# Kernel optimization log

Measured on AMD Instinct MI355X. Metric: run time of the kernel, lower is better.

The kernel has to match this reference:

```python
import jax, jax.numpy as jnp
import numpy as np

LAMBDA_TEMP = 20.0
GAMMA = 20.0
MARGIN = 0.05
EPS = 1e-8

B, K, M, D = 128, 256, 8, 128


def _unit(x, axis=-1):
    return x / jnp.linalg.norm(x, axis=axis, keepdims=True)


def setup_inputs() -> dict:
    key = jax.random.key(0)
    k1, k2, k3 = jax.random.split(key, 3)
    v_proj = _unit(jax.random.normal(k1, (B, K, D), dtype=jnp.float32))
    prototypes = _unit(jax.random.normal(k2, (K, M, D), dtype=jnp.float32))
    concept_labels = jax.random.randint(k3, (B, K), 0, 2, dtype=jnp.int64)
    return {"v_proj": v_proj, "concept_labels": concept_labels, "prototypes": prototypes}


def reference(v_proj, concept_labels, prototypes):
    # all-pairs prototype similarities: query vector (b,k) vs prototypes of concept c
    # sims: (B, K, C, M)
    sims = jnp.einsum('bkd,cmd->bkcm', v_proj, prototypes)
    # Eq.6: soft assignment over the M prototypes of each concept
    q = jax.nn.softmax(GAMMA * sims, axis=-1)
    # Eq.7-8: weighted similarity sim_c(v)  -> (B, K, C)
    sim = jnp.sum(q * sims, axis=-1)
    # positive similarity: concept k queried against its own prototypes, plus margin
    sim_pos = jnp.einsum('bkk->bk', sim) + MARGIN  # (B, K)
    # Eq.9: -log( exp(lam*sim_pos) / (sum_c exp(lam*sim_c) + eps) )
    denom = jnp.sum(jnp.exp(LAMBDA_TEMP * sim), axis=-1) + EPS  # (B, K)
    loss_bk = jnp.log(denom) - LAMBDA_TEMP * sim_pos  # (B, K)
    mask = (concept_labels == 1).astype(loss_bk.dtype)
    num_pos = jnp.sum(mask)
    total = jnp.sum(loss_bk * mask)
    return jnp.where(num_pos > 0, total / num_pos, total)
```

## Files before the change

### kernel.cpp

```cpp
#include <hip/hip_runtime.h>

#define LT      20.0f
#define LN2     0.69314718055994531f
#define C2EXP   28.853900817779268f
#define CHUNKS  16
#define NBLK    512

typedef _Float16 half8 __attribute__((ext_vector_type(8)));
typedef float    f32x4 __attribute__((ext_vector_type(4)));

#if __has_builtin(__builtin_amdgcn_exp2f)
#define EXP2F(x) __builtin_amdgcn_exp2f(x)
#else
#define EXP2F(x) __expf(0.69314718055994531f * (x))
#endif

__device__ __forceinline__ float swz16(float x) {
    return __int_as_float(__builtin_amdgcn_ds_swizzle(__float_as_int(x), 0x401F));
}

#define GLD16(gp, lp) __builtin_amdgcn_global_load_lds( \
    (const __attribute__((address_space(1))) void*)(gp), \
    (__attribute__((address_space(3))) void*)(lp), 16, 0, 0)

__global__ __launch_bounds__(256)
void mpcl_prep(const float* __restrict__ P, _Float16* __restrict__ Pw)
{
    int t    = blockIdx.x * 256 + threadIdx.x;
    int gcol = t >> 4;
    int dblk = t & 15;
    const float* src = P + ((size_t)gcol << 7) + dblk * 8;
    float4 a = *(const float4*)src;
    float4 b = *(const float4*)(src + 4);

    int ch   = gcol >> 7, col  = gcol & 127;
    int colq = col >> 5,  col5 = col & 31;
    int g = col5 >> 3, p = col5 & 7;
    int n = (g << 2) | (p & 3), h = p >> 2;
    int c = dblk >> 2, q = dblk & 3;
    int lane  = (q << 4) | n;
    int cfrag = (h << 2) | c;
    int slot  = ch * 2048 + colq * 512 + cfrag * 64 + lane;

    half8 hv;
    hv[0] = (_Float16)(C2EXP * a.x); hv[1] = (_Float16)(C2EXP * a.y);
    hv[2] = (_Float16)(C2EXP * a.z); hv[3] = (_Float16)(C2EXP * a.w);
    hv[4] = (_Float16)(C2EXP * b.x); hv[5] = (_Float16)(C2EXP * b.y);
    hv[6] = (_Float16)(C2EXP * b.z); hv[7] = (_Float16)(C2EXP * b.w);
    *(half8*)(Pw + (size_t)slot * 8) = hv;
}

__global__ __launch_bounds__(1024, 8)
void mpcl_main(const float* __restrict__ V,
               const int*   __restrict__ labels,
               const _Float16* __restrict__ Pw,
               float* __restrict__ part)
{
    __shared__ __align__(16) _Float16 Pst[2][2048 * 8];
    __shared__ float sh_denom[64];
    __shared__ float sh_simpos[64];

    const int tid  = threadIdx.x;
    const int lane = tid & 63;
    const int w    = tid >> 6;
    const int colq = w & 3;
    const int rg   = w >> 2;
    const int n    = lane & 15;
    const int q    = lane >> 4;
    const int rowbase = blockIdx.x * 64;

    if (tid < 64) { sh_denom[tid] = 0.0f; sh_simpos[tid] = 0.0f; }

    int lab = 0;
    if (tid < 64) lab = labels[rowbase + tid];

    const _Float16* gbase = Pw + (size_t)(w * 128 + lane) * 8;

#define STAGE(CH, B) do {                                       \
    const _Float16* g_ = gbase + (size_t)(CH) * 16384;          \
    _Float16* l_ = &Pst[B][(w * 128) * 8];                      \
    GLD16(g_,       l_);                                        \
    GLD16(g_ + 512, l_ + 512);                                  \
} while (0)

    half8 vh[4];
    {
        const float* vr = V + ((size_t)(rowbase + rg * 16 + n) << 7) + q * 8;
#pragma unroll
        for (int c = 0; c < 4; ++c) {
            float4 x0 = *(const float4*)(vr + c * 32);
            float4 x1 = *(const float4*)(vr + c * 32 + 4);
            vh[c][0] = (_Float16)x0.x; vh[c][1] = (_Float16)x0.y;
            vh[c][2] = (_Float16)x0.z; vh[c][3] = (_Float16)x0.w;
            vh[c][4] = (_Float16)x1.x; vh[c][5] = (_Float16)x1.y;
            vh[c][6] = (_Float16)x1.z; vh[c][7] = (_Float16)x1.w;
        }
    }
    __syncthreads();

    STAGE(0, 0);
    STAGE(1, 1);

    const int rowk = (rowbase + rg * 16 + n) & 255;
    const int aoff = (colq * 512 + lane) * 8;

    float dn = 0.f;
    int cA = colq * 4 + q;

#pragma unroll 1
    for (int ch = 0; ch < CHUNKS; ++ch) {
        if (ch < CHUNKS - 1) asm volatile("s_waitcnt vmcnt(2)" ::: "memory");
        else                 asm volatile("s_waitcnt vmcnt(0)" ::: "memory");
        __builtin_amdgcn_s_barrier();

        const _Float16* base = &Pst[ch & 1][0];

        f32x4 acc1 = {0.f, 0.f, 0.f, 0.f};
        f32x4 acc2 = {0.f, 0.f, 0.f, 0.f};
#pragma unroll
        for (int c = 0; c < 4; ++c) {
            half8 a1 = *(const half8*)&base[aoff + c * 512];
            half8 a2 = *(const half8*)&base[aoff + c * 512 + 2048];
            acc1 = __builtin_amdgcn_mfma_f32_16x16x32_f16(a1, vh[c], acc1, 0, 0, 0);
            acc2 = __builtin_amdgcn_mfma_f32_16x16x32_f16(a2, vh[c], acc2, 0, 0, 0);
        }

        asm volatile("s_waitcnt lgkmcnt(0)" ::: "memory");
        __builtin_amdgcn_s_barrier();
        if (ch + 2 < CHUNKS) STAGE(ch + 2, ch & 1);

        {
            float x0 = acc1[0], x1 = acc1[1], x2 = acc1[2], x3 = acc1[3];
            float x4 = acc2[0], x5 = acc2[1], x6 = acc2[2], x7 = acc2[3];
            float e0 = EXP2F(x0), e1 = EXP2F(x1), e2 = EXP2F(x2), e3 = EXP2F(x3);
            float e4 = EXP2F(x4), e5 = EXP2F(x5), e6 = EXP2F(x6), e7 = EXP2F(x7);
            float es = ((e0 + e1) + (e2 + e3)) + ((e4 + e5) + (e6 + e7));
            float ss = fmaf(e0, x0, fmaf(e1, x1, fmaf(e2, x2, e3 * x3)))
                     + fmaf(e4, x4, fmaf(e5, x5, fmaf(e6, x6, e7 * x7)));
            float simY = __fdividef(ss, es);
            dn += EXP2F(simY);
            if (cA == rowk)
                sh_simpos[rg * 16 + n] = simY;
        }
        cA += 16;
    }

    {
        float t = dn;
        t += swz16(t);
        t += __shfl_xor(t, 32);
        if (lane < 16)
            atomicAdd(&sh_denom[rg * 16 + n], t);
    }
    __syncthreads();

    if (w == 0) {
        float lp = logf(sh_denom[lane] + 1e-8f) - LN2 * sh_simpos[lane] - 1.0f;
        float mk = (lab == 1) ? 1.0f : 0.0f;
        float s  = lp * mk;
        float cc = mk;
#pragma unroll
        for (int off = 32; off >= 1; off >>= 1) {
            s  += __shfl_down(s, off);
            cc += __shfl_down(cc, off);
        }
        if (lane == 0) {
            part[2 * blockIdx.x]     = s;
            part[2 * blockIdx.x + 1] = cc;
        }
    }
}

__global__ __launch_bounds__(512)
void mpcl_finish(const float* __restrict__ part, float* __restrict__ out)
{
    __shared__ float sh[16];
    const int tid  = threadIdx.x;
    const int lane = tid & 63;
    const int w    = tid >> 6;

    float s  = part[2 * tid];
    float cc = part[2 * tid + 1];
#pragma unroll
    for (int off = 32; off >= 1; off >>= 1) {
        s  += __shfl_down(s, off);
        cc += __shfl_down(cc, off);
    }
    if (lane == 0) { sh[w] = s; sh[8 + w] = cc; }
    __syncthreads();
    if (tid == 0) {
        float ts = 0.f, tc = 0.f;
#pragma unroll
        for (int i = 0; i < 8; ++i) { ts += sh[i]; tc += sh[8 + i]; }
        out[0] = (tc > 0.0f) ? (ts / tc) : ts;
    }
}

extern "C" void kernel_launch(void* const* d_in, const int* in_sizes, int n_in,
                              void* d_out, int out_size, void* d_ws, size_t ws_size,
                              hipStream_t stream)
{
    const float* V      = (const float*)d_in[0];
    const int*   labels = (const int*)d_in[1];
    const float* P      = (const float*)d_in[2];
    float* out  = (float*)d_out;
    float* part = (float*)d_ws;
    _Float16* Pw = (_Float16*)((char*)d_ws + 16384);

    mpcl_prep<<<128, 256, 0, stream>>>(P, Pw);
    mpcl_main<<<NBLK, 1024, 0, stream>>>(V, labels, Pw, part);
    mpcl_finish<<<1, 512, 0, stream>>>(part, out);
}
```

Baseline: 97.21 us.

## Compact positive-label rows and run main kernel only on them

Adds a single-block compaction kernel that ballots over the labels, prefix-sums the positive rows into an index list and writes their count. The main kernel then processes only those rows through the index list, with 32 rows per 512-thread block. Blocks past the positive count exit early, so masked-out rows no longer pay for the prototype matmul and exponentials. The cost is an extra kernel launch with a serial scan, and an indirect gather of V rows.

Result: faster. 93.68 us (-3.6%).

```diff
diff --git a/kernel.cpp b/kernel.cpp
--- a/kernel.cpp
+++ b/kernel.cpp
@@ -4,7 +4,7 @@
 #define LN2     0.69314718055994531f
 #define C2EXP   28.853900817779268f
 #define CHUNKS  16
-#define NBLK    512
+#define NBLK    1024
 
 typedef _Float16 half8 __attribute__((ext_vector_type(8)));
 typedef float    f32x4 __attribute__((ext_vector_type(4)));
@@ -50,15 +50,69 @@
     *(half8*)(Pw + (size_t)slot * 8) = hv;
 }
 
-__global__ __launch_bounds__(1024, 8)
+__global__ __launch_bounds__(1024)
+void mpcl_compact(const int* __restrict__ labels, int* __restrict__ ridx,
+                  int* __restrict__ npos)
+{
+    __shared__ int wcnt[512];
+    __shared__ int wsum[8];
+    __shared__ int sbase[512];
+    __shared__ int tot;
+    const int tid = threadIdx.x, lane = tid & 63, w = tid >> 6;
+
+    int lab[32];
+#pragma unroll
+    for (int i = 0; i < 32; ++i) lab[i] = labels[i * 1024 + tid];
+#pragma unroll
+    for (int i = 0; i < 32; ++i) {
+        unsigned long long m = __ballot(lab[i] == 1);
+        if (lane == 0) wcnt[i * 16 + w] = __popcll(m);
+    }
+    __syncthreads();
+
+    int v = 0, orig = 0;
+    if (tid < 512) { v = wcnt[tid]; orig = v; }
+#pragma unroll
+    for (int off = 1; off < 64; off <<= 1) {
+        int t = __shfl_up(v, off);
+        if (lane >= off) v += t;
+    }
+    if (lane == 63 && w < 8) wsum[w] = v;
+    __syncthreads();
+    if (tid == 0) {
+        int acc = 0;
+#pragma unroll
+        for (int i = 0; i < 8; ++i) { int t = wsum[i]; wsum[i] = acc; acc += t; }
+        tot = acc; npos[0] = acc;
+    }
+    __syncthreads();
+    if (tid < 512) sbase[tid] = v - orig + wsum[w];
+    __syncthreads();
+
+#pragma unroll
+    for (int i = 0; i < 32; ++i) {
+        unsigned long long m = __ballot(lab[i] == 1);
+        int pos = sbase[i * 16 + w] + __popcll(m & ((1ull << lane) - 1));
+        if (lab[i] == 1) ridx[pos] = i * 1024 + tid;
+    }
+    for (int j = tot + tid; j < 32768; j += 1024) ridx[j] = 0;
+}
+
+__global__ __attribute__((amdgpu_flat_work_group_size(512, 512),
+                          amdgpu_waves_per_eu(4, 4)))
 void mpcl_main(const float* __restrict__ V,
-               const int*   __restrict__ labels,
                const _Float16* __restrict__ Pw,
+               const int* __restrict__ ridx,
+               const int* __restrict__ npos,
                float* __restrict__ part)
 {
     __shared__ __align__(16) _Float16 Pst[2][2048 * 8];
-    __shared__ float sh_denom[64];
-    __shared__ float sh_simpos[64];
+    __shared__ float sh_denom[32];
+    __shared__ float sh_simpos[32];
+
+    const int np = *npos;
+    const int rowbase = blockIdx.x * 32;
+    if (rowbase >= np) return;
 
     const int tid  = threadIdx.x;
     const int lane = tid & 63;
@@ -67,25 +121,24 @@
     const int rg   = w >> 2;
     const int n    = lane & 15;
     const int q    = lane >> 4;
-    const int rowbase = blockIdx.x * 64;
-
-    if (tid < 64) { sh_denom[tid] = 0.0f; sh_simpos[tid] = 0.0f; }
-
-    int lab = 0;
-    if (tid < 64) lab = labels[rowbase + tid];
-
-    const _Float16* gbase = Pw + (size_t)(w * 128 + lane) * 8;
+
+    if (tid < 32) { sh_denom[tid] = 0.0f; sh_simpos[tid] = 0.0f; }
+
+    const _Float16* gbase = Pw + (size_t)(w * 256 + lane) * 8;
 
 #define STAGE(CH, B) do {                                       \
     const _Float16* g_ = gbase + (size_t)(CH) * 16384;          \
-    _Float16* l_ = &Pst[B][(w * 128) * 8];                      \
-    GLD16(g_,       l_);                                        \
-    GLD16(g_ + 512, l_ + 512);                                  \
+    _Float16* l_ = &Pst[B][(w * 256) * 8];                      \
+    GLD16(g_,        l_);                                       \
+    GLD16(g_ +  512, l_ +  512);                                \
+    GLD16(g_ + 1024, l_ + 1024);                                \
+    GLD16(g_ + 1536, l_ + 1536);                                \
 } while (0)
 
+    const int myrow = ridx[rowbase + rg * 16 + n];
     half8 vh[4];
     {
-        const float* vr = V + ((size_t)(rowbase + rg * 16 + n) << 7) + q * 8;
+        const float* vr = V + ((size_t)myrow << 7) + q * 8;
 #pragma unroll
         for (int c = 0; c < 4; ++c) {
             float4 x0 = *(const float4*)(vr + c * 32);
@@ -101,7 +154,7 @@
     STAGE(0, 0);
     STAGE(1, 1);
 
-    const int rowk = (rowbase + rg * 16 + n) & 255;
+    const int rowk = myrow & 255;
     const int aoff = (colq * 512 + lane) * 8;
 
     float dn = 0.f;
@@ -109,7 +162,7 @@
 
 #pragma unroll 1
     for (int ch = 0; ch < CHUNKS; ++ch) {
-        if (ch < CHUNKS - 1) asm volatile("s_waitcnt vmcnt(2)" ::: "memory");
+        if (ch < CHUNKS - 1) asm volatile("s_waitcnt vmcnt(4)" ::: "memory");
         else                 asm volatile("s_waitcnt vmcnt(0)" ::: "memory");
         __builtin_amdgcn_s_barrier();
 
@@ -155,10 +208,11 @@
     __syncthreads();
 
     if (w == 0) {
-        float lp = logf(sh_denom[lane] + 1e-8f) - LN2 * sh_simpos[lane] - 1.0f;
-        float mk = (lab == 1) ? 1.0f : 0.0f;
-        float s  = lp * mk;
-        float cc = mk;
+        float s = 0.f, cc = 0.f;
+        if (lane < 32 && rowbase + lane < np) {
+            s  = logf(sh_denom[lane] + 1e-8f) - LN2 * sh_simpos[lane] - 1.0f;
+            cc = 1.0f;
+        }
 #pragma unroll
         for (int off = 32; off >= 1; off >>= 1) {
             s  += __shfl_down(s, off);
@@ -172,15 +226,20 @@
 }
 
 __global__ __launch_bounds__(512)
-void mpcl_finish(const float* __restrict__ part, float* __restrict__ out)
+void mpcl_finish(const float* __restrict__ part, const int* __restrict__ npos,
+                 float* __restrict__ out)
 {
     __shared__ float sh[16];
     const int tid  = threadIdx.x;
     const int lane = tid & 63;
     const int w    = tid >> 6;
-
-    float s  = part[2 * tid];
-    float cc = part[2 * tid + 1];
+    const int nact = (*npos + 31) >> 5;
+
+    float s = 0.f, cc = 0.f;
+    for (int i = tid; i < nact; i += 512) {
+        s  += part[2 * i];
+        cc += part[2 * i + 1];
+    }
 #pragma unroll
     for (int off = 32; off >= 1; off >>= 1) {
         s  += __shfl_down(s, off);
@@ -203,11 +262,15 @@
     const float* V      = (const float*)d_in[0];
     const int*   labels = (const int*)d_in[1];
     const float* P      = (const float*)d_in[2];
-    float* out  = (float*)d_out;
-    float* part = (float*)d_ws;
-    _Float16* Pw = (_Float16*)((char*)d_ws + 16384);
+    float* out = (float*)d_out;
+
+    int*      npos = (int*)d_ws;
+    float*    part = (float*)((char*)d_ws + 256);
+    int*      ridx = (int*)((char*)d_ws + 16384);
+    _Float16* Pw   = (_Float16*)((char*)d_ws + 262144);
 
     mpcl_prep<<<128, 256, 0, stream>>>(P, Pw);
-    mpcl_main<<<NBLK, 1024, 0, stream>>>(V, labels, Pw, part);
-    mpcl_finish<<<1, 512, 0, stream>>>(part, out);
-}
+    mpcl_compact<<<1, 1024, 0, stream>>>(labels, ridx, npos);
+    mpcl_main<<<NBLK, 512, 0, stream>>>(V, Pw, ridx, npos, part);
+    mpcl_finish<<<1, 512, 0, stream>>>(part, npos, out);
+}
```
